# Optimization experiments

Hardware: AMD Instinct MI355X
Metric: run time of the kernel (lower is better)

The kernel has to match this reference:

```python
import jax, jax.numpy as jnp
import numpy as np

B, T, H, W = 4, 1024, 27, 48
LOOKUP = 101          # must be odd
OUT_DIM = 128
NBINS = 512           # 8 levels per RGB channel -> 8^3


def setup_inputs() -> dict:
    key = jax.random.key(0)
    k1, k2 = jax.random.split(key, 2)
    frames = jax.random.randint(k1, (B, T, H, W, 3), 0, 256, dtype=jnp.int32)
    # nn.Linear(lookup_window, output_dim): weight [out,in] in torch; store transposed [in,out]
    bound = 1.0 / np.sqrt(LOOKUP)
    fc_w = jax.random.uniform(k2, (LOOKUP, OUT_DIM), jnp.float32, -bound, bound)
    fc_b = jnp.zeros((OUT_DIM,), dtype=jnp.float32)
    return {"frames": frames, "fc_w": fc_w, "fc_b": fc_b}


def _color_histograms(frames):
    b, t, h, w, _ = frames.shape
    flat = frames.reshape(b * t, h * w, 3)
    # bit-pack RGB into 9-bit bin id: (R>>5)<<6 | (G>>5)<<3 | (B>>5)
    bins = ((flat[..., 0] >> 5) << 6) + ((flat[..., 1] >> 5) << 3) + (flat[..., 2] >> 5)
    bins = bins + (jnp.arange(b * t, dtype=jnp.int32) << 9)[:, None]  # per-frame offset
    hist = jax.ops.segment_sum(
        jnp.ones((b * t * h * w,), jnp.float32),
        bins.reshape(-1),
        num_segments=b * t * NBINS,
    ).reshape(b, t, NBINS)
    # F.normalize(p=2, dim=2): x / max(||x||, eps)
    norm = jnp.sqrt(jnp.sum(hist * hist, axis=2, keepdims=True))
    return hist / jnp.maximum(norm, 1e-12)


def reference(frames, fc_w, fc_b):
    x = _color_histograms(frames)             # [b, t, 512]
    b, t, _ = x.shape
    sims = jnp.einsum('bic,bjc->bij', x, x)   # [b, t, t]
    pad = (LOOKUP - 1) // 2
    sims_pad = jnp.pad(sims, ((0, 0), (0, 0), (pad, pad)))  # [b, t, t+L-1]
    # windowed gather: out[b,i,j] = sims_pad[b, i, i+j]
    row = jnp.arange(t)[:, None]                     # [t, 1]
    col = row + jnp.arange(LOOKUP)[None, :]          # [t, L]
    win = sims_pad[:, row, col]                      # [b, t, L]
    return jax.nn.relu(jnp.einsum('btl,lo->bto', win, fc_w) + fc_b)
```

## Files before the change

### kernel.cpp

```cpp
#include <hip/hip_runtime.h>
#include <math.h>

#define NB 4
#define NT 1024
#define NPIX 1296
#define NBINS 512
#define LOOKUP 101
#define PADW 50
#define ODIM 128
#define TT 4
#define WROWS (TT + 2 * PADW)

typedef _Float16 v2h __attribute__((ext_vector_type(2)));

__device__ inline float dot2(unsigned a, unsigned b, float acc) {
    union U { unsigned u; v2h h; } ua, ub;
    ua.u = a; ub.u = b;
#if __has_builtin(__builtin_amdgcn_fdot2)
    return __builtin_amdgcn_fdot2(ua.h, ub.h, acc, false);
#else
    return acc + (float)ua.h.x * (float)ub.h.x + (float)ua.h.y * (float)ub.h.y;
#endif
}

__global__ __launch_bounds__(256) void hist_kernel(const int* __restrict__ frames,
                                                   unsigned short* __restrict__ X) {
    const int wv = threadIdx.x >> 6;
    const int lane = threadIdx.x & 63;
    const int frame = blockIdx.x * 4 + wv;

    __shared__ unsigned int hist[4][NBINS];
    unsigned int* h = hist[wv];

#pragma unroll
    for (int k = 0; k < NBINS / 64; ++k) h[lane + 64 * k] = 0u;

    const int4* f4 = (const int4*)(frames + (size_t)frame * NPIX * 3);
    for (int g = lane; g < NPIX / 4; g += 64) {
        int4 a = f4[g * 3 + 0];
        int4 b = f4[g * 3 + 1];
        int4 c = f4[g * 3 + 2];
        int v[12] = {a.x, a.y, a.z, a.w, b.x, b.y, b.z, b.w, c.x, c.y, c.z, c.w};
#pragma unroll
        for (int p = 0; p < 4; ++p) {
            int bin = ((v[3 * p] >> 5) << 6) | ((v[3 * p + 1] >> 5) << 3) | (v[3 * p + 2] >> 5);
            atomicAdd(&h[bin], 1u);
        }
    }

    float cnt[8];
    float local = 0.f;
#pragma unroll
    for (int k = 0; k < 8; ++k) {
        cnt[k] = (float)h[lane + 64 * k];
        local += cnt[k] * cnt[k];
    }
    for (int off = 32; off >= 1; off >>= 1) local += __shfl_xor(local, off, 64);
    float inv = 1.0f / fmaxf(sqrtf(local), 1e-12f);

    unsigned short* xr = X + (size_t)frame * NBINS;
#pragma unroll
    for (int k = 0; k < 8; ++k) {
        union { _Float16 h16; unsigned short u; } cv;
        cv.h16 = (_Float16)(cnt[k] * inv);
        xr[lane + 64 * k] = cv.u;
    }
}

__global__ __launch_bounds__(256) void simsfc_kernel(const unsigned short* __restrict__ X,
                                                     const float* __restrict__ w,
                                                     const float* __restrict__ bias,
                                                     float* __restrict__ out) {
    const int bid = blockIdx.x;
    const int tile = ((bid & 7) << 7) | (bid >> 3);
    const int b = tile >> 8;
    const int t0 = (tile & 255) * TT;
    const int tid = threadIdx.x;
    const int gid = tid >> 4;
    const int kl = tid & 15;

    __shared__ __align__(16) uint4 st[TT][64];
    __shared__ float win_s[TT][LOOKUP + 3];

    const uint4* Xb4 = (const uint4*)(X + (size_t)b * NT * NBINS);

    {
        int dt = tid >> 6, col = tid & 63;
        st[dt][col] = Xb4[(size_t)(t0 + dt) * 64 + col];
    }
    for (int i = tid; i < TT * (LOOKUP + 3); i += 256) ((float*)win_s)[i] = 0.f;
    __syncthreads();

    uint4 tA[TT][4];
#pragma unroll
    for (int dt = 0; dt < TT; ++dt)
#pragma unroll
        for (int i = 0; i < 4; ++i) tA[dt][i] = st[dt][kl + 16 * i];

    for (int it = 0; it < 7; ++it) {
        const int joff = it * 16 + gid;
        if (joff >= WROWS) continue;
        const int j = t0 - PADW + joff;
        if (j < 0 || j >= NT) continue;
        uint4 A[4];
        const uint4* xj = Xb4 + (size_t)j * 64;
#pragma unroll
        for (int i = 0; i < 4; ++i) A[i] = xj[kl + 16 * i];
#pragma unroll
        for (int dt = 0; dt < TT; ++dt) {
            float s = 0.f;
#pragma unroll
            for (int i = 0; i < 4; ++i) {
                s = dot2(A[i].x, tA[dt][i].x, s);
                s = dot2(A[i].y, tA[dt][i].y, s);
                s = dot2(A[i].z, tA[dt][i].z, s);
                s = dot2(A[i].w, tA[dt][i].w, s);
            }
            s += __shfl_xor(s, 1, 64);
            s += __shfl_xor(s, 2, 64);
            s += __shfl_xor(s, 4, 64);
            s += __shfl_xor(s, 8, 64);
            const int l = joff - dt;
            if (kl == 0 && (unsigned)l <= 100u) win_s[dt][l] = s;
        }
    }
    __syncthreads();

    const int ch = tid & 127;
    const int g2 = tid >> 7;
    float acc0 = bias[ch], acc1 = acc0;
#pragma unroll 4
    for (int l = 0; l < LOOKUP; ++l) {
        float wv = w[l * ODIM + ch];
        acc0 = fmaf(win_s[g2][l], wv, acc0);
        acc1 = fmaf(win_s[g2 + 2][l], wv, acc1);
    }
    float* o0 = out + ((size_t)(b * NT + t0 + g2) * ODIM) + ch;
    o0[0] = fmaxf(acc0, 0.f);
    o0[2 * ODIM] = fmaxf(acc1, 0.f);
}

extern "C" void kernel_launch(void* const* d_in, const int* in_sizes, int n_in,
                              void* d_out, int out_size, void* d_ws, size_t ws_size,
                              hipStream_t stream) {
    const int*   frames = (const int*)d_in[0];
    const float* fc_w   = (const float*)d_in[1];
    const float* fc_b   = (const float*)d_in[2];
    float* out = (float*)d_out;

    unsigned short* X = (unsigned short*)d_ws;

    hist_kernel  <<<NB * NT / 4, 256, 0, stream>>>(frames, X);
    simsfc_kernel<<<NB * NT / TT, 256, 0, stream>>>(X, fc_w, fc_b, out);
}
```

Baseline: 113.8 us.

## Compute windowed similarities with MFMA 16x16x32 f16 tiles per 16-row block

Replaces the per-thread fdot2 similarity loop with MFMA 16x16x32 f16 instructions. Each block now handles 16 query frames, and 8 wavefronts cover 128 candidate frames, which spans the 116-wide window. Out-of-range candidates are clamped for loading and zeroed on write. The FC stage switches to float4 weight loads with one row per 32 threads, and the block grows to 512 threads. Some MFMA output is wasted on columns outside the band, and global operand loads are no longer staged through shared memory.

New measurement: 113.1 us. Within noise of the previous version (-0.6%).

```diff
diff --git a/kernel.cpp b/kernel.cpp
--- a/kernel.cpp
+++ b/kernel.cpp
@@ -8,20 +8,12 @@
 #define LOOKUP 101
 #define PADW 50
 #define ODIM 128
-#define TT 4
-#define WROWS (TT + 2 * PADW)
+#define MT 16
+#define NWIN 116
+#define WPAD 104
 
-typedef _Float16 v2h __attribute__((ext_vector_type(2)));
-
-__device__ inline float dot2(unsigned a, unsigned b, float acc) {
-    union U { unsigned u; v2h h; } ua, ub;
-    ua.u = a; ub.u = b;
-#if __has_builtin(__builtin_amdgcn_fdot2)
-    return __builtin_amdgcn_fdot2(ua.h, ub.h, acc, false);
-#else
-    return acc + (float)ua.h.x * (float)ub.h.x + (float)ua.h.y * (float)ub.h.y;
-#endif
-}
+typedef _Float16 v8h __attribute__((ext_vector_type(8)));
+typedef float v4f __attribute__((ext_vector_type(4)));
 
 __global__ __launch_bounds__(256) void hist_kernel(const int* __restrict__ frames,
                                                    unsigned short* __restrict__ X) {
@@ -67,77 +59,60 @@
     }
 }
 
-__global__ __launch_bounds__(256) void simsfc_kernel(const unsigned short* __restrict__ X,
+__global__ __launch_bounds__(512) void simsfc_kernel(const unsigned short* __restrict__ Xu,
                                                      const float* __restrict__ w,
                                                      const float* __restrict__ bias,
                                                      float* __restrict__ out) {
     const int bid = blockIdx.x;
-    const int tile = ((bid & 7) << 7) | (bid >> 3);
-    const int b = tile >> 8;
-    const int t0 = (tile & 255) * TT;
+    const int tile = ((bid & 7) << 5) | (bid >> 3);
+    const int b = tile >> 6;
+    const int t0 = (tile & 63) * MT;
     const int tid = threadIdx.x;
-    const int gid = tid >> 4;
-    const int kl = tid & 15;
+    const int L = tid & 63;
+    const int ntile = tid >> 6;
 
-    __shared__ __align__(16) uint4 st[TT][64];
-    __shared__ float win_s[TT][LOOKUP + 3];
+    const _Float16* Xh = (const _Float16*)Xu + (size_t)b * NT * NBINS;
 
-    const uint4* Xb4 = (const uint4*)(X + (size_t)b * NT * NBINS);
+    __shared__ float win_s[MT][WPAD];
 
-    {
-        int dt = tid >> 6, col = tid & 63;
-        st[dt][col] = Xb4[(size_t)(t0 + dt) * 64 + col];
+    const _Float16* Ap = Xh + (size_t)(t0 + (L & 15)) * NBINS + 8 * (L >> 4);
+    const int n = ntile * 16 + (L & 15);
+    const int jl = t0 - PADW + n;
+    const int jc = min(max(jl, 0), NT - 1);
+    const _Float16* Bp = Xh + (size_t)jc * NBINS + 8 * (L >> 4);
+
+    v4f acc = {0.f, 0.f, 0.f, 0.f};
+#pragma unroll
+    for (int s = 0; s < 16; ++s) {
+        v8h a = *(const v8h*)(Ap + 32 * s);
+        v8h bb = *(const v8h*)(Bp + 32 * s);
+        acc = __builtin_amdgcn_mfma_f32_16x16x32_f16(a, bb, acc, 0, 0, 0);
     }
-    for (int i = tid; i < TT * (LOOKUP + 3); i += 256) ((float*)win_s)[i] = 0.f;
-    __syncthreads();
 
-    uint4 tA[TT][4];
+    const bool jvalid = (jl >= 0) && (jl < NT);
 #pragma unroll
-    for (int dt = 0; dt < TT; ++dt)
-#pragma unroll
-        for (int i = 0; i < 4; ++i) tA[dt][i] = st[dt][kl + 16 * i];
-
-    for (int it = 0; it < 7; ++it) {
-        const int joff = it * 16 + gid;
-        if (joff >= WROWS) continue;
-        const int j = t0 - PADW + joff;
-        if (j < 0 || j >= NT) continue;
-        uint4 A[4];
-        const uint4* xj = Xb4 + (size_t)j * 64;
-#pragma unroll
-        for (int i = 0; i < 4; ++i) A[i] = xj[kl + 16 * i];
-#pragma unroll
-        for (int dt = 0; dt < TT; ++dt) {
-            float s = 0.f;
-#pragma unroll
-            for (int i = 0; i < 4; ++i) {
-                s = dot2(A[i].x, tA[dt][i].x, s);
-                s = dot2(A[i].y, tA[dt][i].y, s);
-                s = dot2(A[i].z, tA[dt][i].z, s);
-                s = dot2(A[i].w, tA[dt][i].w, s);
-            }
-            s += __shfl_xor(s, 1, 64);
-            s += __shfl_xor(s, 2, 64);
-            s += __shfl_xor(s, 4, 64);
-            s += __shfl_xor(s, 8, 64);
-            const int l = joff - dt;
-            if (kl == 0 && (unsigned)l <= 100u) win_s[dt][l] = s;
-        }
+    for (int r = 0; r < 4; ++r) {
+        const int m = 4 * (L >> 4) + r;
+        const int l = n - m;
+        if ((unsigned)l <= 100u) win_s[m][l] = jvalid ? acc[r] : 0.f;
     }
     __syncthreads();
 
-    const int ch = tid & 127;
-    const int g2 = tid >> 7;
-    float acc0 = bias[ch], acc1 = acc0;
+    const int m = tid >> 5;
+    const int ch = (tid & 31) * 4;
+    v4f a4 = *(const v4f*)(bias + ch);
 #pragma unroll 4
     for (int l = 0; l < LOOKUP; ++l) {
-        float wv = w[l * ODIM + ch];
-        acc0 = fmaf(win_s[g2][l], wv, acc0);
-        acc1 = fmaf(win_s[g2 + 2][l], wv, acc1);
+        float wl = win_s[m][l];
+        v4f wv = *(const v4f*)(w + l * ODIM + ch);
+        a4.x = fmaf(wl, wv.x, a4.x);
+        a4.y = fmaf(wl, wv.y, a4.y);
+        a4.z = fmaf(wl, wv.z, a4.z);
+        a4.w = fmaf(wl, wv.w, a4.w);
     }
-    float* o0 = out + ((size_t)(b * NT + t0 + g2) * ODIM) + ch;
-    o0[0] = fmaxf(acc0, 0.f);
-    o0[2 * ODIM] = fmaxf(acc1, 0.f);
+    a4.x = fmaxf(a4.x, 0.f); a4.y = fmaxf(a4.y, 0.f);
+    a4.z = fmaxf(a4.z, 0.f); a4.w = fmaxf(a4.w, 0.f);
+    *(v4f*)(out + (size_t)(b * NT + t0 + m) * ODIM + ch) = a4;
 }
 
 extern "C" void kernel_launch(void* const* d_in, const int* in_sizes, int n_in,
@@ -151,5 +126,5 @@
     unsigned short* X = (unsigned short*)d_ws;
 
     hist_kernel  <<<NB * NT / 4, 256, 0, stream>>>(frames, X);
-    simsfc_kernel<<<NB * NT / TT, 256, 0, stream>>>(X, fc_w, fc_b, out);
+    simsfc_kernel<<<NB * NT / MT, 512, 0, stream>>>(X, fc_w, fc_b, out);
 }
```
